# Kernel optimization log

Measured on AMD Instinct MI355X. Metric: run time of the kernel, lower is better.

Reference implementation:

```python
import jax, jax.numpy as jnp
import numpy as np

H = 4  # hidden_size
I = 2  # input_size
T = 50  # seq_len
B = 262144  # batch
OUT = 1


def _lstm_layer(x, Wih, Whh, bih, bhh):
    # x: [T, B, in]; PyTorch gate order i, f, g, o in rows of Wih/Whh.
    b = bih + bhh
    h0 = jnp.zeros((x.shape[1], Whh.shape[1]), x.dtype)
    c0 = jnp.zeros_like(h0)

    def step(carry, xt):
        h, c = carry
        gates = xt @ Wih.T + h @ Whh.T + b  # [B, 4H]
        i, f, g, o = jnp.split(gates, 4, axis=-1)
        c = jax.nn.sigmoid(f) * c + jax.nn.sigmoid(i) * jnp.tanh(g)
        h = jax.nn.sigmoid(o) * jnp.tanh(c)
        return (h, c), h

    (_, _), ys = jax.lax.scan(step, (h0, c0), x)
    return ys  # [T, B, H]


def setup_inputs() -> dict:
    key = jax.random.key(0)
    ks = jax.random.split(key, 11)
    s = 1.0 / np.sqrt(H)  # PyTorch LSTM/Linear init scale
    u = lambda k, shp: jax.random.uniform(k, shp, jnp.float32, -s, s)
    x = jax.random.normal(ks[0], (B, T, I), jnp.float32)
    return {
        "x": x,
        "Wih0": u(ks[1], (4 * H, I)),
        "Whh0": u(ks[2], (4 * H, H)),
        "bih0": u(ks[3], (4 * H,)),
        "bhh0": u(ks[4], (4 * H,)),
        "Wih1": u(ks[5], (4 * H, H)),
        "Whh1": u(ks[6], (4 * H, H)),
        "bih1": u(ks[7], (4 * H,)),
        "bhh1": u(ks[8], (4 * H,)),
        "Wout": jax.random.uniform(ks[9], (OUT, H * T), jnp.float32, -1.0 / np.sqrt(H * T), 1.0 / np.sqrt(H * T)),
        "bout": jax.random.uniform(ks[10], (OUT,), jnp.float32, -1.0 / np.sqrt(H * T), 1.0 / np.sqrt(H * T)),
    }


def reference(x, Wih0, Whh0, bih0, bhh0, Wih1, Whh1, bih1, bhh1, Wout, bout):
    xt = jnp.transpose(x, (1, 0, 2))  # [T, B, I]
    y = _lstm_layer(xt, Wih0, Whh0, bih0, bhh0)  # [T, B, H]
    y = _lstm_layer(y, Wih1, Whh1, bih1, bhh1)   # [T, B, H]
    y = jnp.transpose(y, (1, 0, 2)).reshape(x.shape[0], -1)  # [B, T*H]
    return jax.nn.sigmoid(y @ Wout.T + bout)  # [B, 1]
```

## Files before the change

kernel.cpp:

```cpp
#include <hip/hip_runtime.h>

#define T_LEN 50
#define I_IN 2

typedef __fp16 fp16x8 __attribute__((ext_vector_type(8)));
typedef float f32x4 __attribute__((ext_vector_type(4)));
typedef unsigned int uint4v __attribute__((ext_vector_type(4)));

__device__ __forceinline__ float EXP2(float x){ return __builtin_amdgcn_exp2f(x); }
__device__ __forceinline__ float RCP(float x){ return __builtin_amdgcn_rcpf(x); }
__device__ __forceinline__ unsigned PKU(float a, float b){
    return __builtin_bit_cast(unsigned, __builtin_amdgcn_cvt_pkrtz(a, b));
}

__device__ __forceinline__ void act(const f32x4 gt, float& c, float& h){
    const float S2 = -2.8853900817779268f;
    const float p = EXP2(gt[0]);
    const float r = EXP2(gt[1]);
    const float q = EXP2(gt[2]);
    const float s = EXP2(gt[3]);
    const float A  = 1.0f + r;
    const float BC = (1.0f + p) * (1.0f + q);
    const float num = fmaf(c, BC, (1.0f - q) * A);
    c = num * RCP(A * BC);
    const float u = EXP2(fminf(c * S2, 96.0f));
    h = (1.0f - u) * RCP((1.0f + s) * (1.0f + u));
}

__global__ __launch_bounds__(256, 8) void lstm_mfma(
    const float* __restrict__ x,
    const float* __restrict__ Wih0, const float* __restrict__ Whh0,
    const float* __restrict__ bih0, const float* __restrict__ bhh0,
    const float* __restrict__ Wih1, const float* __restrict__ Whh1,
    const float* __restrict__ bih1, const float* __restrict__ bhh1,
    const float* __restrict__ Wout, const float* __restrict__ bout,
    float* __restrict__ out, int B)
{
    __shared__ float wout_s[T_LEN*4];
    const int tid = threadIdx.x;
    if (tid < T_LEN*4) wout_s[tid] = Wout[tid];
    __syncthreads();

    const int lane = tid & 63;
    const int e = lane & 15;
    const int g = lane >> 4;
    const bool g0 = (g == 0);
    const int wave = (blockIdx.x * 256 + tid) >> 6;
    const int E0 = wave * 16;
    if (E0 >= B) return;

    const float S1 = -1.4426950408889634f;
    const float S2 = -2.8853900817779268f;

    const int ja = e >> 2, ta = e & 3;
    const int ra = ta*4 + ja;
    const float sa = (ta == 2) ? S2 : S1;

    uint4v a0u, a1u;
#pragma unroll
    for (int p_ = 0; p_ < 4; ++p_){
        float v[2][2];
#pragma unroll
        for (int h_ = 0; h_ < 2; ++h_){
            const int k = 8*g + 2*p_ + h_;
            float v0 = 0.f, v1 = 0.f;
            if (k < 2)      v0 = Wih0[ra*2 + k] * sa;
            else if (k < 6) v0 = Whh0[ra*4 + (k-2)] * sa;
            if (k < 4)      v1 = Wih1[ra*4 + k] * sa;
            else if (k < 8) v1 = Whh1[ra*4 + (k-4)] * sa;
            v[h_][0] = v0; v[h_][1] = v1;
        }
        a0u[p_] = PKU(v[0][0], v[1][0]);
        a1u[p_] = PKU(v[0][1], v[1][1]);
    }
    const fp16x8 A0 = __builtin_bit_cast(fp16x8, a0u);
    const fp16x8 A1 = __builtin_bit_cast(fp16x8, a1u);

    f32x4 bias0, bias1;
#pragma unroll
    for (int t = 0; t < 4; ++t){
        const int r = t*4 + g;
        const float st = (t == 2) ? S2 : S1;
        bias0[t] = (bih0[r] + bhh0[r]) * st;
        bias1[t] = (bih1[r] + bhh1[r]) * st;
    }

    float c0 = 0.f, c1 = 0.f, acc = 0.f;
    unsigned hp0 = 0u, hp1 = 0u;
    unsigned hr0 = 0u, hr1 = 0u;

    const float* xp = x + (size_t)(E0 + e) * (T_LEN*I_IN);

    for (int tt = 0; tt < T_LEN/2; ++tt){
        const float4 xv = *reinterpret_cast<const float4*>(xp + tt*4);
#pragma unroll
        for (int hh = 0; hh < 2; ++hh){
            const float x0 = hh ? xv.z : xv.x;
            const float x1 = hh ? xv.w : xv.y;
            const unsigned ux = g0 ? PKU(x0, x1) : 0u;

            uint4v b0u; b0u[0] = ux; b0u[1] = hp0; b0u[2] = hp1; b0u[3] = 0u;
            const f32x4 gt0 = __builtin_amdgcn_mfma_f32_16x16x32_f16(
                A0, __builtin_bit_cast(fp16x8, b0u), bias0, 0, 0, 0);
            float h0;
            act(gt0, c0, h0);

            {
                const float p0 = __shfl(h0, e,      64);
                const float p1 = __shfl(h0, e + 16, 64);
                const float p2 = __shfl(h0, e + 32, 64);
                const float p3 = __shfl(h0, e + 48, 64);
                hp0 = g0 ? PKU(p0, p1) : 0u;
                hp1 = g0 ? PKU(p2, p3) : 0u;
            }

            uint4v b1u; b1u[0] = hp0; b1u[1] = hp1; b1u[2] = hr0; b1u[3] = hr1;
            const f32x4 gt1 = __builtin_amdgcn_mfma_f32_16x16x32_f16(
                A1, __builtin_bit_cast(fp16x8, b1u), bias1, 0, 0, 0);
            float h1;
            act(gt1, c1, h1);

            {
                const float q0 = __shfl(h1, e,      64);
                const float q1 = __shfl(h1, e + 16, 64);
                const float q2 = __shfl(h1, e + 32, 64);
                const float q3 = __shfl(h1, e + 48, 64);
                hr0 = g0 ? PKU(q0, q1) : 0u;
                hr1 = g0 ? PKU(q2, q3) : 0u;
            }

            acc = fmaf(h1, wout_s[(2*tt + hh)*4 + g], acc);
        }
    }

    acc += __shfl_xor(acc, 16, 64);
    acc += __shfl_xor(acc, 32, 64);

    if (lane < 16){
        const float z = acc + bout[0];
        out[E0 + e] = RCP(1.0f + EXP2(z * S1));
    }
}

extern "C" void kernel_launch(void* const* d_in, const int* in_sizes, int n_in,
                              void* d_out, int out_size, void* d_ws, size_t ws_size,
                              hipStream_t stream)
{
    const float* x    = (const float*)d_in[0];
    const float* Wih0 = (const float*)d_in[1];
    const float* Whh0 = (const float*)d_in[2];
    const float* bih0 = (const float*)d_in[3];
    const float* bhh0 = (const float*)d_in[4];
    const float* Wih1 = (const float*)d_in[5];
    const float* Whh1 = (const float*)d_in[6];
    const float* bih1 = (const float*)d_in[7];
    const float* bhh1 = (const float*)d_in[8];
    const float* Wout = (const float*)d_in[9];
    const float* bout = (const float*)d_in[10];
    float* out = (float*)d_out;

    const int B = in_sizes[0] / (T_LEN*I_IN);
    const int waves = (B + 15) / 16;
    const int blocks = (waves + 3) / 4;
    lstm_mfma<<<blocks, 256, 0, stream>>>(x, Wih0, Whh0, bih0, bhh0,
                                          Wih1, Whh1, bih1, bhh1,
                                          Wout, bout, out, B);
}
```

Before: 109.2 us.

## Fuse both LSTM layers into one skewed 32x32 MFMA per timestep

Replaces the two 16x16x32 MFMAs per step (one per layer) with a single 32x32x16 MFMA. Layer 0 at step t and layer 1 at step t-1 are computed together in a wavefront-skewed schedule, with a prologue and an epilogue step. Each wave now handles 32 batch elements instead of 16, and the lane shuffles become cheap xor-32 exchanges. The goals are to halve the serial MFMA-to-activation dependency chain per timestep and to cut shuffle overhead. In exchange, each lane does four activations per step, register pressure rises, and occupancy bounds drop to 4.

```diff
diff --git a/kernel.cpp b/kernel.cpp
--- a/kernel.cpp
+++ b/kernel.cpp
@@ -1,10 +1,9 @@
 #include <hip/hip_runtime.h>
 
 #define T_LEN 50
-#define I_IN 2
 
 typedef __fp16 fp16x8 __attribute__((ext_vector_type(8)));
-typedef float f32x4 __attribute__((ext_vector_type(4)));
+typedef float f32x16 __attribute__((ext_vector_type(16)));
 typedef unsigned int uint4v __attribute__((ext_vector_type(4)));
 
 __device__ __forceinline__ float EXP2(float x){ return __builtin_amdgcn_exp2f(x); }
@@ -13,12 +12,13 @@
     return __builtin_bit_cast(unsigned, __builtin_amdgcn_cvt_pkrtz(a, b));
 }
 
-__device__ __forceinline__ void act(const f32x4 gt, float& c, float& h){
+__device__ __forceinline__ void act(float gi, float gf, float gg, float go,
+                                    float& c, float& h){
     const float S2 = -2.8853900817779268f;
-    const float p = EXP2(gt[0]);
-    const float r = EXP2(gt[1]);
-    const float q = EXP2(gt[2]);
-    const float s = EXP2(gt[3]);
+    const float p = EXP2(gi);
+    const float r = EXP2(gf);
+    const float q = EXP2(gg);
+    const float s = EXP2(go);
     const float A  = 1.0f + r;
     const float BC = (1.0f + p) * (1.0f + q);
     const float num = fmaf(c, BC, (1.0f - q) * A);
@@ -27,7 +27,7 @@
     h = (1.0f - u) * RCP((1.0f + s) * (1.0f + u));
 }
 
-__global__ __launch_bounds__(256, 8) void lstm_mfma(
+__global__ __launch_bounds__(256, 4) void lstm_mfma32(
     const float* __restrict__ x,
     const float* __restrict__ Wih0, const float* __restrict__ Whh0,
     const float* __restrict__ bih0, const float* __restrict__ bhh0,
@@ -36,107 +36,119 @@
     const float* __restrict__ Wout, const float* __restrict__ bout,
     float* __restrict__ out, int B)
 {
-    __shared__ float wout_s[T_LEN*4];
+    __shared__ float2 wout_s[T_LEN*2];
     const int tid = threadIdx.x;
-    if (tid < T_LEN*4) wout_s[tid] = Wout[tid];
+    if (tid < T_LEN*2){
+        const int t = tid >> 1, hh = tid & 1;
+        wout_s[tid] = make_float2(Wout[t*4+hh], Wout[t*4+hh+2]);
+    }
     __syncthreads();
 
     const int lane = tid & 63;
-    const int e = lane & 15;
-    const int g = lane >> 4;
-    const bool g0 = (g == 0);
-    const int wave = (blockIdx.x * 256 + tid) >> 6;
-    const int E0 = wave * 16;
+    const int e = lane & 31;
+    const int h = lane >> 5;
+    const int wave = (blockIdx.x*256 + tid) >> 6;
+    const int E0 = wave * 32;
     if (E0 >= B) return;
 
     const float S1 = -1.4426950408889634f;
     const float S2 = -2.8853900817779268f;
 
-    const int ja = e >> 2, ta = e & 3;
-    const int ra = ta*4 + ja;
-    const float sa = (ta == 2) ? S2 : S1;
+    const int qA = e >> 2, tA = e & 3;
+    const float sA = (tA == 2) ? S2 : S1;
+    uint4v au;
+#pragma unroll
+    for (int p = 0; p < 4; ++p){
+        float vv[2];
+#pragma unroll
+        for (int z = 0; z < 2; ++z){
+            const int k = 8*h + 2*p + z;
+            float v = 0.f;
+            if (qA < 4){
+                const int r = tA*4 + qA;
+                if (k < 2)      v = Wih0[r*2 + k];
+                else if (k < 6) v = Whh0[r*4 + (k-2)];
+            } else {
+                const int r = tA*4 + (qA-4);
+                if (k >= 2 && k < 6)       v = Wih1[r*4 + (k-2)];
+                else if (k >= 6 && k < 10) v = Whh1[r*4 + (k-6)];
+            }
+            vv[z] = v * sA;
+        }
+        au[p] = PKU(vv[0], vv[1]);
+    }
+    const fp16x8 Afrag = __builtin_bit_cast(fp16x8, au);
 
-    uint4v a0u, a1u;
+    f32x16 biasC;
 #pragma unroll
-    for (int p_ = 0; p_ < 4; ++p_){
-        float v[2][2];
-#pragma unroll
-        for (int h_ = 0; h_ < 2; ++h_){
-            const int k = 8*g + 2*p_ + h_;
-            float v0 = 0.f, v1 = 0.f;
-            if (k < 2)      v0 = Wih0[ra*2 + k] * sa;
-            else if (k < 6) v0 = Whh0[ra*4 + (k-2)] * sa;
-            if (k < 4)      v1 = Wih1[ra*4 + k] * sa;
-            else if (k < 8) v1 = Whh1[ra*4 + (k-4)] * sa;
-            v[h_][0] = v0; v[h_][1] = v1;
-        }
-        a0u[p_] = PKU(v[0][0], v[1][0]);
-        a1u[p_] = PKU(v[0][1], v[1][1]);
-    }
-    const fp16x8 A0 = __builtin_bit_cast(fp16x8, a0u);
-    const fp16x8 A1 = __builtin_bit_cast(fp16x8, a1u);
-
-    f32x4 bias0, bias1;
-#pragma unroll
-    for (int t = 0; t < 4; ++t){
-        const int r = t*4 + g;
-        const float st = (t == 2) ? S2 : S1;
-        bias0[t] = (bih0[r] + bhh0[r]) * st;
-        bias1[t] = (bih1[r] + bhh1[r]) * st;
+    for (int r = 0; r < 16; ++r){
+        const int m = (r&3) + 8*(r>>2) + 4*h;
+        const int q = m >> 2, tg = m & 3;
+        const float st = (tg == 2) ? S2 : S1;
+        if (q < 4){ const int rr = tg*4 + q;      biasC[r] = (bih0[rr]+bhh0[rr])*st; }
+        else      { const int rr = tg*4 + (q-4);  biasC[r] = (bih1[rr]+bhh1[rr])*st; }
     }
 
-    float c0 = 0.f, c1 = 0.f, acc = 0.f;
-    unsigned hp0 = 0u, hp1 = 0u;
-    unsigned hr0 = 0u, hr1 = 0u;
+    float c0l=0.f, c0h=0.f, c1l=0.f, c1h=0.f, acc=0.f;
+    unsigned pk_h0_01=0u, pk_h0_23=0u, pk_h1_01=0u, pk_h1_23=0u;
 
-    const float* xp = x + (size_t)(E0 + e) * (T_LEN*I_IN);
+    const float* xp = x + (size_t)(E0 + e) * (T_LEN*2);
 
-    for (int tt = 0; tt < T_LEN/2; ++tt){
-        const float4 xv = *reinterpret_cast<const float4*>(xp + tt*4);
-#pragma unroll
-        for (int hh = 0; hh < 2; ++hh){
-            const float x0 = hh ? xv.z : xv.x;
-            const float x1 = hh ? xv.w : xv.y;
-            const unsigned ux = g0 ? PKU(x0, x1) : 0u;
-
-            uint4v b0u; b0u[0] = ux; b0u[1] = hp0; b0u[2] = hp1; b0u[3] = 0u;
-            const f32x4 gt0 = __builtin_amdgcn_mfma_f32_16x16x32_f16(
-                A0, __builtin_bit_cast(fp16x8, b0u), bias0, 0, 0, 0);
-            float h0;
-            act(gt0, c0, h0);
-
-            {
-                const float p0 = __shfl(h0, e,      64);
-                const float p1 = __shfl(h0, e + 16, 64);
-                const float p2 = __shfl(h0, e + 32, 64);
-                const float p3 = __shfl(h0, e + 48, 64);
-                hp0 = g0 ? PKU(p0, p1) : 0u;
-                hp1 = g0 ? PKU(p2, p3) : 0u;
-            }
-
-            uint4v b1u; b1u[0] = hp0; b1u[1] = hp1; b1u[2] = hr0; b1u[3] = hr1;
-            const f32x4 gt1 = __builtin_amdgcn_mfma_f32_16x16x32_f16(
-                A1, __builtin_bit_cast(fp16x8, b1u), bias1, 0, 0, 0);
-            float h1;
-            act(gt1, c1, h1);
-
-            {
-                const float q0 = __shfl(h1, e,      64);
-                const float q1 = __shfl(h1, e + 16, 64);
-                const float q2 = __shfl(h1, e + 32, 64);
-                const float q3 = __shfl(h1, e + 48, 64);
-                hr0 = g0 ? PKU(q0, q1) : 0u;
-                hr1 = g0 ? PKU(q2, q3) : 0u;
-            }
-
-            acc = fmaf(h1, wout_s[(2*tt + hh)*4 + g], acc);
-        }
+    {
+        const float2 xv = *reinterpret_cast<const float2*>(xp);
+        const unsigned ux = PKU(xv.x, xv.y);
+        uint4v bu; bu[0] = h ? 0u : ux; bu[1] = 0u; bu[2] = 0u; bu[3] = 0u;
+        const f32x16 d = __builtin_amdgcn_mfma_f32_32x32x16_f16(
+            Afrag, __builtin_bit_cast(fp16x8, bu), biasC, 0, 0, 0);
+        float h0l, h0h;
+        act(d[0],d[1],d[2],d[3], c0l, h0l);
+        act(d[4],d[5],d[6],d[7], c0h, h0h);
+        const float r0l = __shfl_xor(h0l, 32, 64);
+        const float r0h = __shfl_xor(h0h, 32, 64);
+        pk_h0_01 = PKU(h0l, r0l);
+        pk_h0_23 = PKU(h0h, r0h);
     }
 
-    acc += __shfl_xor(acc, 16, 64);
+    for (int t = 1; t < T_LEN; ++t){
+        const float2 xv = *reinterpret_cast<const float2*>(xp + t*2);
+        const unsigned ux = PKU(xv.x, xv.y);
+        uint4v bu;
+        bu[0] = h ? pk_h1_23 : ux;
+        bu[1] = pk_h0_01;
+        bu[2] = pk_h0_23;
+        bu[3] = pk_h1_01;
+        const f32x16 d = __builtin_amdgcn_mfma_f32_32x32x16_f16(
+            Afrag, __builtin_bit_cast(fp16x8, bu), biasC, 0, 0, 0);
+        float h0l,h0h,h1l,h1h;
+        act(d[0], d[1], d[2], d[3],  c0l, h0l);
+        act(d[4], d[5], d[6], d[7],  c0h, h0h);
+        act(d[8], d[9], d[10],d[11], c1l, h1l);
+        act(d[12],d[13],d[14],d[15], c1h, h1h);
+        const float2 wo = wout_s[(t-1)*2 + h];
+        acc = fmaf(h1l, wo.x, fmaf(h1h, wo.y, acc));
+        const float r0l = __shfl_xor(h0l,32,64), r0h = __shfl_xor(h0h,32,64);
+        const float r1l = __shfl_xor(h1l,32,64), r1h = __shfl_xor(h1h,32,64);
+        pk_h0_01 = PKU(h0l, r0l);
+        pk_h0_23 = PKU(h0h, r0h);
+        pk_h1_01 = PKU(h1l, r1l);
+        pk_h1_23 = PKU(r1h, h1h);
+    }
+
+    {
+        uint4v bu;
+        bu[0] = h ? pk_h1_23 : 0u;
+        bu[1] = pk_h0_01; bu[2] = pk_h0_23; bu[3] = pk_h1_01;
+        const f32x16 d = __builtin_amdgcn_mfma_f32_32x32x16_f16(
+            Afrag, __builtin_bit_cast(fp16x8, bu), biasC, 0, 0, 0);
+        float h1l, h1h;
+        act(d[8], d[9], d[10],d[11], c1l, h1l);
+        act(d[12],d[13],d[14],d[15], c1h, h1h);
+        const float2 wo = wout_s[49*2 + h];
+        acc = fmaf(h1l, wo.x, fmaf(h1h, wo.y, acc));
+    }
+
     acc += __shfl_xor(acc, 32, 64);
-
-    if (lane < 16){
+    if (h == 0){
         const float z = acc + bout[0];
         out[E0 + e] = RCP(1.0f + EXP2(z * S1));
     }
@@ -159,10 +171,10 @@
     const float* bout = (const float*)d_in[10];
     float* out = (float*)d_out;
 
-    const int B = in_sizes[0] / (T_LEN*I_IN);
-    const int waves = (B + 15) / 16;
+    const int B = in_sizes[0] / (T_LEN*2);
+    const int waves = (B + 31) / 32;
     const int blocks = (waves + 3) / 4;
-    lstm_mfma<<<blocks, 256, 0, stream>>>(x, Wih0, Whh0, bih0, bhh0,
-                                          Wih1, Whh1, bih1, bhh1,
-                                          Wout, bout, out, B);
+    lstm_mfma32<<<blocks, 256, 0, stream>>>(x, Wih0, Whh0, bih0, bhh0,
+                                            Wih1, Whh1, bih1, bhh1,
+                                            Wout, bout, out, B);
 }
```

Result: slower. 117.4 us (+7.5%).
